# Kernel tuning notes

Measured on AMD Instinct MI355X. Metric: run time of the kernel, lower is better.

## Reference

```python
import jax, jax.numpy as jnp
import numpy as np

N = 100000      # nodes
E = 1600000     # edges (avg degree 16)
D_IN = 64
H1, H2, OUT = 64, 32, 2


def setup_inputs() -> dict:
    key = jax.random.key(0)
    ks = jax.random.split(key, 12)
    x = jax.random.normal(ks[0], (N, D_IN), jnp.float32)
    edge_index = jax.random.randint(ks[1], (2, E), 0, N, dtype=jnp.int32)

    def lin(k, fin, fout):
        return jax.random.normal(k, (fin, fout), jnp.float32) / np.sqrt(fin)

    return {
        "x": x,
        "edge_index": edge_index,
        # SAGEConv1: lin_l (neighbors, with bias) + lin_r (root, no bias)
        "Wl1": lin(ks[2], D_IN, H1), "bl1": jnp.zeros((H1,), jnp.float32),
        "Wr1": lin(ks[3], D_IN, H1),
        # SAGEConv2
        "Wl2": lin(ks[4], H1, H2), "bl2": jnp.zeros((H2,), jnp.float32),
        "Wr2": lin(ks[5], H1, H2),
        # final Linear(32, 2)
        "Wf": lin(ks[6], H2, OUT),
        "bf": jnp.zeros((OUT,), jnp.float32),
    }


def reference(x, edge_index, Wl1, bl1, Wr1, Wl2, bl2, Wr2, Wf, bf):
    src, dst = edge_index[0], edge_index[1]
    n = x.shape[0]
    # in-degree for mean aggregation (isolated nodes -> divide by 1, aggr stays 0)
    deg = jax.ops.segment_sum(jnp.ones(src.shape, x.dtype), dst, num_segments=n)
    inv_deg = 1.0 / jnp.maximum(deg, 1.0)

    def sage(h, Wl, bl, Wr):
        # gather source features, scatter-sum to targets, then mean
        aggr = jax.ops.segment_sum(h[src], dst, num_segments=n) * inv_deg[:, None]
        return aggr @ Wl + bl + h @ Wr  # lin_l(mean_neigh) + lin_r(root)

    h = jax.nn.relu(sage(x, Wl1, bl1, Wr1))
    h = jax.nn.relu(sage(h, Wl2, bl2, Wr2))
    return h @ Wf + bf
```

## Files before the change

### kernel.cpp

```cpp
#include <hip/hip_runtime.h>

#define NN 100000
#define EE 1600000
#define NB 391
#define BCAP 4608
#define BINB 640
#define EPB (EE / BINB)
#define NL1B ((NN + 63) / 64)
#define NPREP 3125
#define PGRID (NPREP + 45)

typedef unsigned int u32;
typedef unsigned short u16;
typedef __attribute__((ext_vector_type(8))) short bf16x8;
typedef __attribute__((ext_vector_type(4))) float f32x4;

__device__ __forceinline__ u32 f2bf(float f) {
    u32 u = __float_as_uint(f);
    return (u + 0x7fffu + ((u >> 16) & 1u)) >> 16;
}
__device__ __forceinline__ float bf_lo(u32 u) { return __uint_as_float(u << 16); }
__device__ __forceinline__ float bf_hi(u32 u) { return __uint_as_float(u & 0xffff0000u); }
__device__ __forceinline__ u32 pk2(float lo, float hi) { return f2bf(lo) | (f2bf(hi) << 16); }

__global__ __launch_bounds__(512) void kbin(const int* __restrict__ src,
                                            const int* __restrict__ dst,
                                            int* __restrict__ gcur,
                                            int* __restrict__ gbin) {
    __shared__ int lsp[EPB];
    __shared__ u16 lsb[EPB];
    __shared__ int ls2[EPB];
    __shared__ int lh[NB + 1];
    __shared__ int lcur[NB];
    __shared__ int lbase[NB];
    int tid = threadIdx.x;
    int e0 = blockIdx.x * EPB;
    for (int t = tid; t < NB; t += 512) { lh[t + 1] = 0; lcur[t] = 0; }
    if (tid == 0) lh[0] = 0;
    __syncthreads();
    for (int i = tid; i < EPB; i += 512) {
        int d = dst[e0 + i], s = src[e0 + i];
        lsp[i] = (s << 8) | (d & 255);
        int b = d >> 8;
        lsb[i] = (u16)b;
        atomicAdd(&lh[b + 1], 1);
    }
    __syncthreads();
    for (int o = 1; o < NB; o <<= 1) {
        int v = 0;
        if (tid < NB && tid >= o) v = lh[tid - o + 1];
        __syncthreads();
        if (tid < NB) lh[tid + 1] += v;
        __syncthreads();
    }
    if (tid < NB) {
        int cnt = lh[tid + 1] - lh[tid];
        lbase[tid] = cnt ? atomicAdd(&gcur[tid], cnt) : 0;
    }
    __syncthreads();
    for (int i = tid; i < EPB; i += 512) {
        int b = lsb[i];
        int pos = atomicAdd(&lcur[b], 1);
        ls2[lh[b] + pos] = lsp[i];
    }
    __syncthreads();
    for (int i = tid; i < EPB; i += 512) {
        int lo = 0, hi = NB - 1;
#pragma unroll
        for (int it = 0; it < 9; ++it) {
            int mid = (lo + hi + 1) >> 1;
            if (lh[mid] <= i) lo = mid; else hi = mid - 1;
        }
        int ib = lbase[lo] + (i - lh[lo]);
        if (ib < BCAP) gbin[(size_t)lo * BCAP + ib] = ls2[i];
    }
}

__global__ __launch_bounds__(512) void ksort(const int* __restrict__ gcur,
                                             const int* __restrict__ gbin,
                                             int* __restrict__ elist,
                                             int* __restrict__ offs,
                                             int* __restrict__ deg) {
    __shared__ int ls[BCAP];
    __shared__ int ls2[BCAP];
    __shared__ int lh0[256], lh[256], lcur[256];
    int tid = threadIdx.x;
    int b = blockIdx.x;
    int cnt = gcur[b]; if (cnt > BCAP) cnt = BCAP;
    const int* bin = gbin + (size_t)b * BCAP;
    for (int i = tid; i < cnt; i += 512) ls[i] = bin[i];
    if (tid < 256) { lh0[tid] = 0; lcur[tid] = 0; }
    __syncthreads();
    for (int i = tid; i < cnt; i += 512) atomicAdd(&lh0[ls[i] & 255], 1);
    __syncthreads();
    if (tid < 256) lh[tid] = lh0[tid];
    __syncthreads();
    for (int o = 1; o < 256; o <<= 1) {
        int v = 0;
        if (tid < 256 && tid >= o) v = lh[tid - o];
        __syncthreads();
        if (tid < 256) lh[tid] += v;
        __syncthreads();
    }
    for (int i = tid; i < cnt; i += 512) {
        int e = ls[i], d = e & 255;
        int pos = atomicAdd(&lcur[d], 1);
        ls2[lh[d] - lh0[d] + pos] = e >> 8;
    }
    __syncthreads();
    int boff = b * BCAP;
    for (int i = tid; i < cnt; i += 512) elist[boff + i] = ls2[i];
    int nodes = NN - b * 256; if (nodes > 256) nodes = 256;
    if (tid < nodes) {
        offs[b * 256 + tid] = boff + lh[tid] - lh0[tid];
        deg[b * 256 + tid] = lh0[tid];
    }
}

__global__ __launch_bounds__(256) void prep_conv(const float* __restrict__ x,
                                                 const float* __restrict__ Wl1,
                                                 const float* __restrict__ Wr1,
                                                 const float* __restrict__ Wl2,
                                                 const float* __restrict__ Wr2,
                                                 u16* __restrict__ xb,
                                                 u16* __restrict__ wbT,
                                                 u16* __restrict__ w2T,
                                                 u32* __restrict__ wr2p,
                                                 u16* __restrict__ z2b,
                                                 int* __restrict__ gcur) {
    int tid = threadIdx.x;
    int b = blockIdx.x;
    if (b < NPREP) {
        int i = b * 256 + tid;
        const float4* x4 = (const float4*)x;
        float4 a = x4[2 * i], c = x4[2 * i + 1];
        ((uint4*)xb)[i] = make_uint4(pk2(a.x, a.y), pk2(a.z, a.w),
                                     pk2(c.x, c.y), pk2(c.z, c.w));
        return;
    }
    int b2 = b - NPREP;
    if (b2 < 32) {
        int idx = b2 * 256 + tid;
        int n = idx >> 7, k = idx & 127;
        float v = (k < 64) ? Wl1[k * 64 + n] : Wr1[(k - 64) * 64 + n];
        wbT[idx] = (u16)f2bf(v);
    } else if (b2 < 40) {
        int idx = (b2 - 32) * 256 + tid;
        int n = idx >> 6, k = idx & 63;
        w2T[idx] = (u16)f2bf(Wl2[k * 32 + n]);
    } else if (b2 < 44) {
        int idx = (b2 - 40) * 256 + tid;
        int k2 = idx >> 5, f = idx & 31;
        wr2p[idx] = pk2(Wr2[(2 * k2) * 32 + f], Wr2[(2 * k2 + 1) * 32 + f]);
    } else {
        for (int t = tid; t < 512; t += 256) gcur[t] = 0;
        if (tid < 32) ((u32*)(xb + (size_t)NN * 64))[tid] = 0;
        else if (tid < 48) ((u32*)(z2b + (size_t)NN * 32))[tid - 32] = 0;
    }
}

__global__ __launch_bounds__(256) void kaggr1(const u16* __restrict__ xb,
                                              const int* __restrict__ offs,
                                              const int* __restrict__ deg,
                                              const int* __restrict__ elist,
                                              u32* __restrict__ aggr1u) {
    int tid = threadIdx.x;
    int l32 = tid & 31;
    int g = tid >> 5;
    int node = blockIdx.x * 8 + g;
    int o0 = offs[node];
    int c = deg[node];
    float inv = 1.0f / fmaxf((float)c, 1.0f);
    if (c > 64) c = 64;
    int e0 = elist[o0 + l32];
    int e1 = elist[o0 + 32 + l32];
    const u32* xbu = (const u32*)xb;
    float aL = 0.f, aH = 0.f;
#define B16A(EREG, JB, CNT)                                                   \
    {                                                                         \
        _Pragma("unroll")                                                     \
        for (int j = 0; j < (CNT); ++j) {                                     \
            int jj = (JB) + j;                                                \
            int id = (jj < c) ? __shfl((EREG), jj & 31, 32) : NN;             \
            u32 u = xbu[(u32)id * 32 + l32];                                  \
            aL += bf_lo(u); aH += bf_hi(u);                                   \
        }                                                                     \
    }
    B16A(e0, 0, 16)
    if (c > 16) B16A(e0, 16, 8)
    if (c > 24) B16A(e0, 24, 8)
    if (c > 32) B16A(e1, 32, 8)
    if (c > 40) B16A(e1, 40, 8)
    if (c > 48) B16A(e1, 48, 8)
    if (c > 56) B16A(e1, 56, 8)
#undef B16A
    aggr1u[(size_t)node * 32 + l32] = pk2(aL * inv, aH * inv);
}

__global__ __launch_bounds__(256) void l1gemm(const u32* __restrict__ aggr1u,
                                              const u16* __restrict__ xb,
                                              const u16* __restrict__ wbT,
                                              const u16* __restrict__ w2T,
                                              const float* __restrict__ bl1,
                                              u16* __restrict__ rh,
                                              u16* __restrict__ z2b) {
    __shared__ u16 sWb[64][136];
    __shared__ u16 sW2[32][72];
    __shared__ u16 sA[64][136];
    __shared__ u16 sH[64][72];
    __shared__ float sbl[64];
    int tid = threadIdx.x;
    int node0 = blockIdx.x * 64;

    for (int idx = tid; idx < 4096; idx += 256) {
        int n = idx >> 6, j = idx & 63;
        ((u32*)&sWb[n][0])[j] = ((const u32*)wbT)[idx];
    }
    for (int idx = tid; idx < 1024; idx += 256) {
        int n = idx >> 5, j = idx & 31;
        ((u32*)&sW2[n][0])[j] = ((const u32*)w2T)[idx];
    }
    if (tid < 64) sbl[tid] = bl1[tid];
    const u32* xbu = (const u32*)xb;
    for (int idx = tid; idx < 2048; idx += 256) {
        int row = idx >> 5, j = idx & 31;
        int nd = node0 + row; if (nd > NN - 1) nd = NN - 1;
        u32* dstA = (u32*)&sA[row][0];
        dstA[j]      = aggr1u[(size_t)nd * 32 + j];
        dstA[32 + j] = xbu[(size_t)nd * 32 + j];
    }
    __syncthreads();

    int l = tid & 63, w = tid >> 6;
    int m = l & 15, sel = l >> 4;

    bf16x8 af[4];
#pragma unroll
    for (int kc = 0; kc < 4; ++kc)
        af[kc] = *(const bf16x8*)&sA[w * 16 + m][kc * 32 + sel * 8];

    f32x4 acc0 = {0.f, 0.f, 0.f, 0.f};
    f32x4 acc1 = acc0, acc2 = acc0, acc3 = acc0;
#pragma unroll
    for (int kc = 0; kc < 4; ++kc) {
        bf16x8 b0 = *(const bf16x8*)&sWb[0 + m][kc * 32 + sel * 8];
        bf16x8 b1 = *(const bf16x8*)&sWb[16 + m][kc * 32 + sel * 8];
        bf16x8 b2 = *(const bf16x8*)&sWb[32 + m][kc * 32 + sel * 8];
        bf16x8 b3 = *(const bf16x8*)&sWb[48 + m][kc * 32 + sel * 8];
        acc0 = __builtin_amdgcn_mfma_f32_16x16x32_bf16(af[kc], b0, acc0, 0, 0, 0);
        acc1 = __builtin_amdgcn_mfma_f32_16x16x32_bf16(af[kc], b1, acc1, 0, 0, 0);
        acc2 = __builtin_amdgcn_mfma_f32_16x16x32_bf16(af[kc], b2, acc2, 0, 0, 0);
        acc3 = __builtin_amdgcn_mfma_f32_16x16x32_bf16(af[kc], b3, acc3, 0, 0, 0);
    }
#pragma unroll
    for (int nt = 0; nt < 4; ++nt) {
        f32x4 a = (nt == 0) ? acc0 : (nt == 1) ? acc1 : (nt == 2) ? acc2 : acc3;
        int col = nt * 16 + m;
        float b = sbl[col];
#pragma unroll
        for (int r = 0; r < 4; ++r) {
            float h = fmaxf(a[r] + b, 0.f);
            sH[w * 16 + sel * 4 + r][col] = (u16)f2bf(h);
        }
    }
    __syncthreads();

    bf16x8 hf0 = *(const bf16x8*)&sH[w * 16 + m][0 + sel * 8];
    bf16x8 hf1 = *(const bf16x8*)&sH[w * 16 + m][32 + sel * 8];
    f32x4 z0 = {0.f, 0.f, 0.f, 0.f};
    f32x4 z1 = z0;
    {
        bf16x8 b00 = *(const bf16x8*)&sW2[0 + m][0 + sel * 8];
        bf16x8 b01 = *(const bf16x8*)&sW2[0 + m][32 + sel * 8];
        bf16x8 b10 = *(const bf16x8*)&sW2[16 + m][0 + sel * 8];
        bf16x8 b11 = *(const bf16x8*)&sW2[16 + m][32 + sel * 8];
        z0 = __builtin_amdgcn_mfma_f32_16x16x32_bf16(hf0, b00, z0, 0, 0, 0);
        z0 = __builtin_amdgcn_mfma_f32_16x16x32_bf16(hf1, b01, z0, 0, 0, 0);
        z1 = __builtin_amdgcn_mfma_f32_16x16x32_bf16(hf0, b10, z1, 0, 0, 0);
        z1 = __builtin_amdgcn_mfma_f32_16x16x32_bf16(hf1, b11, z1, 0, 0, 0);
    }
#pragma unroll
    for (int r = 0; r < 4; ++r) {
        int node = node0 + w * 16 + sel * 4 + r;
        if (node < NN) {
            z2b[(size_t)node * 32 + m]      = (u16)f2bf(z0[r]);
            z2b[(size_t)node * 32 + 16 + m] = (u16)f2bf(z1[r]);
        }
    }
    for (int idx = tid; idx < 2048; idx += 256) {
        int row = idx >> 5, j = idx & 31;
        int node = node0 + row;
        if (node < NN) ((u32*)rh)[(size_t)node * 32 + j] = *(const u32*)&sH[row][2 * j];
    }
}

__global__ __launch_bounds__(256) void kaggr2(const u16* __restrict__ z2b,
                                              const int* __restrict__ offs,
                                              const int* __restrict__ deg,
                                              const int* __restrict__ elist,
                                              u32* __restrict__ aggr2u) {
    int tid = threadIdx.x;
    int l16 = tid & 15;
    int g = tid >> 4;
    int node = blockIdx.x * 16 + g;
    int o0 = offs[node];
    int c = deg[node];
    float inv = 1.0f / fmaxf((float)c, 1.0f);
    if (c > 64) c = 64;
    int e0 = elist[o0 + l16], e1 = elist[o0 + 16 + l16];
    int e2 = elist[o0 + 32 + l16], e3 = elist[o0 + 48 + l16];
    const u32* zu = (const u32*)z2b;
    float aL = 0.f, aH = 0.f;
#define B16B(EREG, JB, CNT)                                                   \
    {                                                                         \
        _Pragma("unroll")                                                     \
        for (int j = 0; j < (CNT); ++j) {                                     \
            int jj = (JB) + j;                                                \
            int id = (jj < c) ? __shfl((EREG), jj & 15, 16) : NN;             \
            u32 u = zu[(u32)id * 16 + l16];                                   \
            aL += bf_lo(u); aH += bf_hi(u);                                   \
        }                                                                     \
    }
    B16B(e0, 0, 16)
    if (c > 16) B16B(e1, 16, 8)
    if (c > 24) B16B(e1, 24, 8)
    if (c > 32) B16B(e2, 32, 8)
    if (c > 40) B16B(e2, 40, 8)
    if (c > 48) B16B(e3, 48, 8)
    if (c > 56) B16B(e3, 56, 8)
#undef B16B
    aggr2u[(size_t)node * 16 + l16] = pk2(aL * inv, aH * inv);
}

__global__ __launch_bounds__(256) void l2gemm(const u16* __restrict__ rh,
                                              const u32* __restrict__ aggr2u,
                                              const u32* __restrict__ wr2p,
                                              const float* __restrict__ bl2,
                                              const float* __restrict__ Wf,
                                              const float* __restrict__ bfin,
                                              float* __restrict__ out) {
    __shared__ u32 sWp[32][32];
    __shared__ float sWf[32][2];
    __shared__ float sh1[16][64];
    __shared__ float sa2[16][32];
    __shared__ float sh2[16][32];
    int tid = threadIdx.x;
    for (int t = tid; t < 1024; t += 256) ((u32*)sWp)[t] = wr2p[t];
    if (tid < 64) sWf[tid >> 1][tid & 1] = Wf[tid];
    const u32* rh32 = (const u32*)rh;
    for (int t = tid; t < 512; t += 256) {
        int g = t >> 5, j = t & 31;
        u32 u = rh32[((size_t)blockIdx.x * 16 + g) * 32 + j];
        sh1[g][2 * j] = bf_lo(u);
        sh1[g][2 * j + 1] = bf_hi(u);
    }
    {
        int g = tid >> 4, j = tid & 15;
        u32 u = aggr2u[((size_t)blockIdx.x * 16 + g) * 16 + j];
        sa2[g][2 * j] = bf_lo(u);
        sa2[g][2 * j + 1] = bf_hi(u);
    }
    __syncthreads();

    int f2 = tid & 31, gg = tid >> 5;
    float b2 = bl2[f2];
    float p0 = sa2[gg][f2] + b2;
    float p1 = sa2[gg + 8][f2] + b2;
#pragma unroll
    for (int k2 = 0; k2 < 32; ++k2) {
        u32 w = sWp[k2][f2];
        float w0 = bf_lo(w), w1 = bf_hi(w);
        float2 aA = *(const float2*)&sh1[gg][2 * k2];
        float2 aB = *(const float2*)&sh1[gg + 8][2 * k2];
        p0 = fmaf(aA.x, w0, p0); p0 = fmaf(aA.y, w1, p0);
        p1 = fmaf(aB.x, w0, p1); p1 = fmaf(aB.y, w1, p1);
    }
    sh2[gg][f2] = fmaxf(p0, 0.f);
    sh2[gg + 8][f2] = fmaxf(p1, 0.f);
    __syncthreads();

    if (tid < 32) {
        int ng = tid >> 1, cc = tid & 1;
        float o = bfin[cc];
#pragma unroll
        for (int k = 0; k < 32; ++k) o = fmaf(sh2[ng][k], sWf[k][cc], o);
        out[((size_t)blockIdx.x * 16 + ng) * 2 + cc] = o;
    }
}

extern "C" void kernel_launch(void* const* d_in, const int* in_sizes, int n_in,
                              void* d_out, int out_size, void* d_ws, size_t ws_size,
                              hipStream_t stream) {
    const float* x   = (const float*)d_in[0];
    const int*   ei  = (const int*)d_in[1];
    const float* Wl1 = (const float*)d_in[2];
    const float* bl1 = (const float*)d_in[3];
    const float* Wr1 = (const float*)d_in[4];
    const float* Wl2 = (const float*)d_in[5];
    const float* bl2 = (const float*)d_in[6];
    const float* Wr2 = (const float*)d_in[7];
    const float* Wf  = (const float*)d_in[8];
    const float* bf  = (const float*)d_in[9];
    float* out = (float*)d_out;

    const int* src = ei;
    const int* dst = ei + EE;

    int*   gcur   = (int*)d_ws;
    int*   deg    = gcur + 512;
    int*   offs   = deg + NN;
    int*   gbin   = offs + NN;
    int*   elist  = gbin + (size_t)NB * BCAP + 64;
    u16*   xb     = (u16*)(elist + (size_t)NB * BCAP + 64);
    u16*   rh     = xb + (size_t)(NN + 1) * 64;
    u16*   z2b    = rh + (size_t)NN * 64;
    u32*   aggr1u = (u32*)(z2b + (size_t)(NN + 1) * 32);
    u16*   wbT    = (u16*)(aggr1u + (size_t)NN * 32);
    u16*   w2T    = wbT + 8192;
    u32*   wr2p   = (u32*)(w2T + 2048);
    u32*   aggr2u = (u32*)gbin;

    prep_conv<<<PGRID, 256, 0, stream>>>(x, Wl1, Wr1, Wl2, Wr2, xb, wbT, w2T, wr2p, z2b, gcur);

    kbin<<<BINB, 512, 0, stream>>>(src, dst, gcur, gbin);

    ksort<<<NB, 512, 0, stream>>>(gcur, gbin, elist, offs, deg);

    kaggr1<<<NN / 8, 256, 0, stream>>>(xb, offs, deg, elist, aggr1u);

    l1gemm<<<NL1B, 256, 0, stream>>>(aggr1u, xb, wbT, w2T, bl1, rh, z2b);

    kaggr2<<<NN / 16, 256, 0, stream>>>(z2b, offs, deg, elist, aggr2u);

    l2gemm<<<NN / 16, 256, 0, stream>>>(rh, aggr2u, wr2p, bl2, Wf, bf, out);
}
```

Measured before the change: 126.2 us.

## Fuse prep into binning kernel and aggr2 into final layer-2 GEMM

Merges the bf16 cast and weight-prep blocks into the edge-binning launch as extra blocks, and replaces the gcur zeroing with a memset. It also fuses the layer-2 neighbour aggregation directly into the final GEMM kernel, keeping the aggregated values in shared memory. This removes two kernel launches and the aggr2 global round trip. In exchange the fused prep blocks carry the binning kernel's large shared-memory footprint, which may limit occupancy, and an extra memset launch is added.

New measurement: 121.0 us. 4.2% less time.

```diff
diff --git a/kernel.cpp b/kernel.cpp
--- a/kernel.cpp
+++ b/kernel.cpp
@@ -7,8 +7,8 @@
 #define BINB 640
 #define EPB (EE / BINB)
 #define NL1B ((NN + 63) / 64)
-#define NPREP 3125
-#define PGRID (NPREP + 45)
+#define XCAST 1563
+#define FGRID (BINB + XCAST + 16 + 4 + 2 + 1)
 
 typedef unsigned int u32;
 typedef unsigned short u16;
@@ -23,10 +23,20 @@
 __device__ __forceinline__ float bf_hi(u32 u) { return __uint_as_float(u & 0xffff0000u); }
 __device__ __forceinline__ u32 pk2(float lo, float hi) { return f2bf(lo) | (f2bf(hi) << 16); }
 
-__global__ __launch_bounds__(512) void kbin(const int* __restrict__ src,
-                                            const int* __restrict__ dst,
-                                            int* __restrict__ gcur,
-                                            int* __restrict__ gbin) {
+__global__ __launch_bounds__(512) void kbinprep(const int* __restrict__ src,
+                                                const int* __restrict__ dst,
+                                                int* __restrict__ gcur,
+                                                int* __restrict__ gbin,
+                                                const float* __restrict__ x,
+                                                const float* __restrict__ Wl1,
+                                                const float* __restrict__ Wr1,
+                                                const float* __restrict__ Wl2,
+                                                const float* __restrict__ Wr2,
+                                                u16* __restrict__ xb,
+                                                u16* __restrict__ wbT,
+                                                u16* __restrict__ w2T,
+                                                u32* __restrict__ wr2p,
+                                                u16* __restrict__ z2b) {
     __shared__ int lsp[EPB];
     __shared__ u16 lsb[EPB];
     __shared__ int ls2[EPB];
@@ -34,45 +44,78 @@
     __shared__ int lcur[NB];
     __shared__ int lbase[NB];
     int tid = threadIdx.x;
-    int e0 = blockIdx.x * EPB;
-    for (int t = tid; t < NB; t += 512) { lh[t + 1] = 0; lcur[t] = 0; }
-    if (tid == 0) lh[0] = 0;
-    __syncthreads();
-    for (int i = tid; i < EPB; i += 512) {
-        int d = dst[e0 + i], s = src[e0 + i];
-        lsp[i] = (s << 8) | (d & 255);
-        int b = d >> 8;
-        lsb[i] = (u16)b;
-        atomicAdd(&lh[b + 1], 1);
-    }
-    __syncthreads();
-    for (int o = 1; o < NB; o <<= 1) {
-        int v = 0;
-        if (tid < NB && tid >= o) v = lh[tid - o + 1];
-        __syncthreads();
-        if (tid < NB) lh[tid + 1] += v;
-        __syncthreads();
-    }
-    if (tid < NB) {
-        int cnt = lh[tid + 1] - lh[tid];
-        lbase[tid] = cnt ? atomicAdd(&gcur[tid], cnt) : 0;
-    }
-    __syncthreads();
-    for (int i = tid; i < EPB; i += 512) {
-        int b = lsb[i];
-        int pos = atomicAdd(&lcur[b], 1);
-        ls2[lh[b] + pos] = lsp[i];
-    }
-    __syncthreads();
-    for (int i = tid; i < EPB; i += 512) {
-        int lo = 0, hi = NB - 1;
-#pragma unroll
-        for (int it = 0; it < 9; ++it) {
-            int mid = (lo + hi + 1) >> 1;
-            if (lh[mid] <= i) lo = mid; else hi = mid - 1;
-        }
-        int ib = lbase[lo] + (i - lh[lo]);
-        if (ib < BCAP) gbin[(size_t)lo * BCAP + ib] = ls2[i];
+    int b = blockIdx.x;
+    if (b < BINB) {
+        int e0 = b * EPB;
+        for (int t = tid; t < NB; t += 512) { lh[t + 1] = 0; lcur[t] = 0; }
+        if (tid == 0) lh[0] = 0;
+        __syncthreads();
+        for (int i = tid; i < EPB; i += 512) {
+            int d = dst[e0 + i], s = src[e0 + i];
+            lsp[i] = (s << 8) | (d & 255);
+            int bb = d >> 8;
+            lsb[i] = (u16)bb;
+            atomicAdd(&lh[bb + 1], 1);
+        }
+        __syncthreads();
+        for (int o = 1; o < NB; o <<= 1) {
+            int v = 0;
+            if (tid < NB && tid >= o) v = lh[tid - o + 1];
+            __syncthreads();
+            if (tid < NB) lh[tid + 1] += v;
+            __syncthreads();
+        }
+        if (tid < NB) {
+            int cnt = lh[tid + 1] - lh[tid];
+            lbase[tid] = cnt ? atomicAdd(&gcur[tid], cnt) : 0;
+        }
+        __syncthreads();
+        for (int i = tid; i < EPB; i += 512) {
+            int bb = lsb[i];
+            int pos = atomicAdd(&lcur[bb], 1);
+            ls2[lh[bb] + pos] = lsp[i];
+        }
+        __syncthreads();
+        for (int i = tid; i < EPB; i += 512) {
+            int lo = 0, hi = NB - 1;
+#pragma unroll
+            for (int it = 0; it < 9; ++it) {
+                int mid = (lo + hi + 1) >> 1;
+                if (lh[mid] <= i) lo = mid; else hi = mid - 1;
+            }
+            int ib = lbase[lo] + (i - lh[lo]);
+            if (ib < BCAP) gbin[(size_t)lo * BCAP + ib] = ls2[i];
+        }
+        return;
+    }
+    int b2 = b - BINB;
+    if (b2 < XCAST) {
+        int i = b2 * 512 + tid;
+        if (i < NN * 64 / 8) {
+            const float4* x4 = (const float4*)x;
+            float4 a = x4[2 * i], c = x4[2 * i + 1];
+            ((uint4*)xb)[i] = make_uint4(pk2(a.x, a.y), pk2(a.z, a.w),
+                                         pk2(c.x, c.y), pk2(c.z, c.w));
+        }
+        return;
+    }
+    b2 -= XCAST;
+    if (b2 < 16) {
+        int idx = b2 * 512 + tid;
+        int n = idx >> 7, k = idx & 127;
+        float v = (k < 64) ? Wl1[k * 64 + n] : Wr1[(k - 64) * 64 + n];
+        wbT[idx] = (u16)f2bf(v);
+    } else if (b2 < 20) {
+        int idx = (b2 - 16) * 512 + tid;
+        int n = idx >> 6, k = idx & 63;
+        w2T[idx] = (u16)f2bf(Wl2[k * 32 + n]);
+    } else if (b2 < 22) {
+        int idx = (b2 - 20) * 512 + tid;
+        int k2 = idx >> 5, f = idx & 31;
+        wr2p[idx] = pk2(Wr2[(2 * k2) * 32 + f], Wr2[(2 * k2 + 1) * 32 + f]);
+    } else {
+        if (tid < 32) ((u32*)(xb + (size_t)NN * 64))[tid] = 0;
+        else if (tid < 48) ((u32*)(z2b + (size_t)NN * 32))[tid - 32] = 0;
     }
 }
 
@@ -114,48 +157,6 @@
     if (tid < nodes) {
         offs[b * 256 + tid] = boff + lh[tid] - lh0[tid];
         deg[b * 256 + tid] = lh0[tid];
-    }
-}
-
-__global__ __launch_bounds__(256) void prep_conv(const float* __restrict__ x,
-                                                 const float* __restrict__ Wl1,
-                                                 const float* __restrict__ Wr1,
-                                                 const float* __restrict__ Wl2,
-                                                 const float* __restrict__ Wr2,
-                                                 u16* __restrict__ xb,
-                                                 u16* __restrict__ wbT,
-                                                 u16* __restrict__ w2T,
-                                                 u32* __restrict__ wr2p,
-                                                 u16* __restrict__ z2b,
-                                                 int* __restrict__ gcur) {
-    int tid = threadIdx.x;
-    int b = blockIdx.x;
-    if (b < NPREP) {
-        int i = b * 256 + tid;
-        const float4* x4 = (const float4*)x;
-        float4 a = x4[2 * i], c = x4[2 * i + 1];
-        ((uint4*)xb)[i] = make_uint4(pk2(a.x, a.y), pk2(a.z, a.w),
-                                     pk2(c.x, c.y), pk2(c.z, c.w));
-        return;
-    }
-    int b2 = b - NPREP;
-    if (b2 < 32) {
-        int idx = b2 * 256 + tid;
-        int n = idx >> 7, k = idx & 127;
-        float v = (k < 64) ? Wl1[k * 64 + n] : Wr1[(k - 64) * 64 + n];
-        wbT[idx] = (u16)f2bf(v);
-    } else if (b2 < 40) {
-        int idx = (b2 - 32) * 256 + tid;
-        int n = idx >> 6, k = idx & 63;
-        w2T[idx] = (u16)f2bf(Wl2[k * 32 + n]);
-    } else if (b2 < 44) {
-        int idx = (b2 - 40) * 256 + tid;
-        int k2 = idx >> 5, f = idx & 31;
-        wr2p[idx] = pk2(Wr2[(2 * k2) * 32 + f], Wr2[(2 * k2 + 1) * 32 + f]);
-    } else {
-        for (int t = tid; t < 512; t += 256) gcur[t] = 0;
-        if (tid < 32) ((u32*)(xb + (size_t)NN * 64))[tid] = 0;
-        else if (tid < 48) ((u32*)(z2b + (size_t)NN * 32))[tid - 32] = 0;
     }
 }
 
@@ -294,51 +295,16 @@
     }
 }
 
-__global__ __launch_bounds__(256) void kaggr2(const u16* __restrict__ z2b,
-                                              const int* __restrict__ offs,
-                                              const int* __restrict__ deg,
-                                              const int* __restrict__ elist,
-                                              u32* __restrict__ aggr2u) {
-    int tid = threadIdx.x;
-    int l16 = tid & 15;
-    int g = tid >> 4;
-    int node = blockIdx.x * 16 + g;
-    int o0 = offs[node];
-    int c = deg[node];
-    float inv = 1.0f / fmaxf((float)c, 1.0f);
-    if (c > 64) c = 64;
-    int e0 = elist[o0 + l16], e1 = elist[o0 + 16 + l16];
-    int e2 = elist[o0 + 32 + l16], e3 = elist[o0 + 48 + l16];
-    const u32* zu = (const u32*)z2b;
-    float aL = 0.f, aH = 0.f;
-#define B16B(EREG, JB, CNT)                                                   \
-    {                                                                         \
-        _Pragma("unroll")                                                     \
-        for (int j = 0; j < (CNT); ++j) {                                     \
-            int jj = (JB) + j;                                                \
-            int id = (jj < c) ? __shfl((EREG), jj & 15, 16) : NN;             \
-            u32 u = zu[(u32)id * 16 + l16];                                   \
-            aL += bf_lo(u); aH += bf_hi(u);                                   \
-        }                                                                     \
-    }
-    B16B(e0, 0, 16)
-    if (c > 16) B16B(e1, 16, 8)
-    if (c > 24) B16B(e1, 24, 8)
-    if (c > 32) B16B(e2, 32, 8)
-    if (c > 40) B16B(e2, 40, 8)
-    if (c > 48) B16B(e3, 48, 8)
-    if (c > 56) B16B(e3, 56, 8)
-#undef B16B
-    aggr2u[(size_t)node * 16 + l16] = pk2(aL * inv, aH * inv);
-}
-
-__global__ __launch_bounds__(256) void l2gemm(const u16* __restrict__ rh,
-                                              const u32* __restrict__ aggr2u,
-                                              const u32* __restrict__ wr2p,
-                                              const float* __restrict__ bl2,
-                                              const float* __restrict__ Wf,
-                                              const float* __restrict__ bfin,
-                                              float* __restrict__ out) {
+__global__ __launch_bounds__(256) void l2fused(const u16* __restrict__ z2b,
+                                               const int* __restrict__ offs,
+                                               const int* __restrict__ deg,
+                                               const int* __restrict__ elist,
+                                               const u16* __restrict__ rh,
+                                               const u32* __restrict__ wr2p,
+                                               const float* __restrict__ bl2,
+                                               const float* __restrict__ Wf,
+                                               const float* __restrict__ bfin,
+                                               float* __restrict__ out) {
     __shared__ u32 sWp[32][32];
     __shared__ float sWf[32][2];
     __shared__ float sh1[16][64];
@@ -354,11 +320,39 @@
         sh1[g][2 * j] = bf_lo(u);
         sh1[g][2 * j + 1] = bf_hi(u);
     }
+
     {
-        int g = tid >> 4, j = tid & 15;
-        u32 u = aggr2u[((size_t)blockIdx.x * 16 + g) * 16 + j];
-        sa2[g][2 * j] = bf_lo(u);
-        sa2[g][2 * j + 1] = bf_hi(u);
+        int l16 = tid & 15;
+        int g = tid >> 4;
+        int node = blockIdx.x * 16 + g;
+        int o0 = offs[node];
+        int c = deg[node];
+        float inv = 1.0f / fmaxf((float)c, 1.0f);
+        if (c > 64) c = 64;
+        int e0 = elist[o0 + l16], e1 = elist[o0 + 16 + l16];
+        int e2 = elist[o0 + 32 + l16], e3 = elist[o0 + 48 + l16];
+        const u32* zu = (const u32*)z2b;
+        float aL = 0.f, aH = 0.f;
+#define B16B(EREG, JB, CNT)                                                   \
+        {                                                                     \
+            _Pragma("unroll")                                                 \
+            for (int j = 0; j < (CNT); ++j) {                                 \
+                int jj = (JB) + j;                                            \
+                int id = (jj < c) ? __shfl((EREG), jj & 15, 16) : NN;         \
+                u32 u = zu[(u32)id * 16 + l16];                               \
+                aL += bf_lo(u); aH += bf_hi(u);                               \
+            }                                                                 \
+        }
+        B16B(e0, 0, 16)
+        if (c > 16) B16B(e1, 16, 8)
+        if (c > 24) B16B(e1, 24, 8)
+        if (c > 32) B16B(e2, 32, 8)
+        if (c > 40) B16B(e2, 40, 8)
+        if (c > 48) B16B(e3, 48, 8)
+        if (c > 56) B16B(e3, 56, 8)
+#undef B16B
+        sa2[g][2 * l16]     = aL * inv;
+        sa2[g][2 * l16 + 1] = aH * inv;
     }
     __syncthreads();
 
@@ -418,11 +412,12 @@
     u16*   wbT    = (u16*)(aggr1u + (size_t)NN * 32);
     u16*   w2T    = wbT + 8192;
     u32*   wr2p   = (u32*)(w2T + 2048);
-    u32*   aggr2u = (u32*)gbin;
-
-    prep_conv<<<PGRID, 256, 0, stream>>>(x, Wl1, Wr1, Wl2, Wr2, xb, wbT, w2T, wr2p, z2b, gcur);
-
-    kbin<<<BINB, 512, 0, stream>>>(src, dst, gcur, gbin);
+
+    hipMemsetAsync(gcur, 0, 512 * sizeof(int), stream);
+
+    kbinprep<<<FGRID, 512, 0, stream>>>(src, dst, gcur, gbin,
+                                        x, Wl1, Wr1, Wl2, Wr2,
+                                        xb, wbT, w2T, wr2p, z2b);
 
     ksort<<<NB, 512, 0, stream>>>(gcur, gbin, elist, offs, deg);
 
@@ -430,7 +425,5 @@
 
     l1gemm<<<NL1B, 256, 0, stream>>>(aggr1u, xb, wbT, w2T, bl1, rh, z2b);
 
-    kaggr2<<<NN / 16, 256, 0, stream>>>(z2b, offs, deg, elist, aggr2u);
-
-    l2gemm<<<NN / 16, 256, 0, stream>>>(rh, aggr2u, wr2p, bl2, Wf, bf, out);
-}
+    l2fused<<<NN / 16, 256, 0, stream>>>(z2b, offs, deg, elist, rh, wr2p, bl2, Wf, bf, out);
+}
```
